# Optimization experiments

Hardware: AMD Instinct MI355X
Metric: run time of the kernel (lower is better)

Reference implementation:

```python
import jax, jax.numpy as jnp
import numpy as np

H = 5  # hidden size of both LSTMs

def _lstm_layer(x, Wih, Whh, bih, bhh):
    """x: [B,T,I] -> hs: [B,T,H]. PyTorch gate order i,f,g,o; zero init state."""
    B, T, _ = x.shape
    # precompute input contribution for all timesteps: [T,B,4H]
    xg = (jnp.einsum('bti,gi->btg', x, Wih) + bih + bhh).transpose(1, 0, 2)
    def step(carry, xg_t):
        h, c = carry
        g = xg_t + h @ Whh.T
        i, f, gg, o = jnp.split(g, 4, axis=-1)
        c = jax.nn.sigmoid(f) * c + jax.nn.sigmoid(i) * jnp.tanh(gg)
        h = jax.nn.sigmoid(o) * jnp.tanh(c)
        return (h, c), h
    h0 = jnp.zeros((B, H), x.dtype)
    (_, _), hs = jax.lax.scan(step, (h0, h0), xg)
    return hs.transpose(1, 0, 2)  # [B,T,H]

def setup_inputs() -> dict:
    key = jax.random.key(0)
    ks = jax.random.split(key, 32)
    B, T = 16384, 128
    def u(k, shape, fan):
        s = 1.0 / np.sqrt(fan)
        return jax.random.uniform(k, shape, jnp.float32, -s, s)
    inp = {
        'x1': jax.random.normal(ks[0], (B, T, 5), jnp.float32),
        'x2': jax.random.normal(ks[1], (B, T, 5), jnp.float32),
        # lstm1 (1 layer)
        'Wih1': u(ks[2], (4*H, 5), H), 'Whh1': u(ks[3], (4*H, H), H),
        'bih1': u(ks[4], (4*H,), H), 'bhh1': u(ks[5], (4*H,), H),
        # lstm2 layer 0
        'Wih2a': u(ks[6], (4*H, 5), H), 'Whh2a': u(ks[7], (4*H, H), H),
        'bih2a': u(ks[8], (4*H,), H), 'bhh2a': u(ks[9], (4*H,), H),
        # lstm2 layer 1
        'Wih2b': u(ks[10], (4*H, H), H), 'Whh2b': u(ks[11], (4*H, H), H),
        'bih2b': u(ks[12], (4*H,), H), 'bhh2b': u(ks[13], (4*H,), H),
        # FC stack 20->32->32->16->16->5
        'W1': u(ks[14], (32, 20), 20), 'b1': u(ks[15], (32,), 20),
        'W2': u(ks[16], (32, 32), 32), 'b2': u(ks[17], (32,), 32),
        'W3': u(ks[18], (16, 32), 32), 'b3': u(ks[19], (16,), 32),
        'W4': u(ks[20], (16, 16), 16), 'b4': u(ks[21], (16,), 16),
        'W5': u(ks[22], (5, 16), 16), 'b5': u(ks[23], (5,), 16),
    }
    return inp

def reference(x1, x2, Wih1, Whh1, bih1, bhh1, Wih2a, Whh2a, bih2a, bhh2a,
              Wih2b, Whh2b, bih2b, bhh2b, W1, b1, W2, b2, W3, b3, W4, b4, W5, b5):
    out1 = _lstm_layer(x1, Wih1, Whh1, bih1, bhh1)[:, -1, :]            # [B,5]
    h2 = _lstm_layer(x2, Wih2a, Whh2a, bih2a, bhh2a)                    # [B,T,5]
    out2 = _lstm_layer(h2, Wih2b, Whh2b, bih2b, bhh2b)[:, -1, :]        # [B,5]
    out = jnp.concatenate([x1[:, -1, :], x2[:, -1, :], out1, out2], axis=1)  # [B,20]
    out = jax.nn.relu(out @ W1.T + b1)
    out = jax.nn.relu(out @ W2.T + b2)
    out = jax.nn.relu(out @ W3.T + b3)
    out = jax.nn.relu(out @ W4.T + b4)
    return out @ W5.T + b5  # [B,5]
```

## Files before the change

### kernel.cpp

```cpp
#include <hip/hip_runtime.h>

#define DEV __device__ __forceinline__
#define KSIG (-1.442695041f)
#define KTANH (-2.885390082f)

typedef float f2 __attribute__((ext_vector_type(2)));

DEV float fexp2(float x) { return __builtin_amdgcn_exp2f(x); }
DEV float frcp(float x) { return __builtin_amdgcn_rcpf(x); }
DEV float bperm(int a, float x) {
  return __int_as_float(__builtin_amdgcn_ds_bpermute(a, __float_as_int(x)));
}
DEV f2 pkfma(f2 a, f2 b, f2 c) { return __builtin_elementwise_fma(a, b, c); }

struct CellP {
  f2 wx[4][2];
  f2 wh[4][2];
  float wx4[4], wh4[4];
  f2 b2[4];
};

DEV void load_cellP(CellP& W, int u, const float* __restrict__ Wih,
                    const float* __restrict__ Whh,
                    const float* __restrict__ bih,
                    const float* __restrict__ bhh) {
#pragma unroll
  for (int rt = 0; rt < 4; ++rt) {
    int row = 5 * rt + u;
    float kx = (rt == 2) ? KTANH : KSIG;
    W.wx[rt][0] = (f2){kx * Wih[row * 5 + 0], kx * Wih[row * 5 + 1]};
    W.wx[rt][1] = (f2){kx * Wih[row * 5 + 2], kx * Wih[row * 5 + 3]};
    W.wx4[rt] = kx * Wih[row * 5 + 4];
    W.wh[rt][0] = (f2){kx * Whh[row * 5 + 0], kx * Whh[row * 5 + 1]};
    W.wh[rt][1] = (f2){kx * Whh[row * 5 + 2], kx * Whh[row * 5 + 3]};
    W.wh4[rt] = kx * Whh[row * 5 + 4];
    W.b2[rt] = (f2){kx * (bih[row] + bhh[row]), 0.f};
  }
}

DEV float stepP(const CellP& W, const f2 xp[2], float x4, float hAll[5],
                float& c, const int bp[5]) {
  f2 hp0 = (f2){hAll[0], hAll[1]};
  f2 hp1 = (f2){hAll[2], hAll[3]};
  float acc[4];
#pragma unroll
  for (int rt = 0; rt < 4; ++rt) {
    f2 a2 = pkfma(W.wx[rt][0], xp[0], W.b2[rt]);
    a2 = pkfma(W.wx[rt][1], xp[1], a2);
    a2 = pkfma(W.wh[rt][0], hp0, a2);
    a2 = pkfma(W.wh[rt][1], hp1, a2);
    float a = a2.x + a2.y;
    a = fmaf(W.wx4[rt], x4, a);
    acc[rt] = fmaf(W.wh4[rt], hAll[4], a);
  }
  float gi = frcp(1.f + fexp2(acc[0]));
  float gf = frcp(1.f + fexp2(acc[1]));
  float gg = fmaf(2.f, frcp(1.f + fexp2(acc[2])), -1.f);
  float go = frcp(1.f + fexp2(acc[3]));
  c = fmaf(gf, c, gi * gg);
  float th = fmaf(2.f, frcp(1.f + fexp2(KTANH * c)), -1.f);
  float h = go * th;
#pragma unroll
  for (int u2 = 0; u2 < 5; ++u2) hAll[u2] = bperm(bp[u2], h);
  return h;
}

__global__ __launch_bounds__(192, 4) void rnn3w_kernel(
    const float* __restrict__ x1, const float* __restrict__ x2,
    const float* __restrict__ Wih1, const float* __restrict__ Whh1,
    const float* __restrict__ bih1, const float* __restrict__ bhh1,
    const float* __restrict__ Wih2a, const float* __restrict__ Whh2a,
    const float* __restrict__ bih2a, const float* __restrict__ bhh2a,
    const float* __restrict__ Wih2b, const float* __restrict__ Whh2b,
    const float* __restrict__ bih2b, const float* __restrict__ bhh2b,
    const float* __restrict__ W1, const float* __restrict__ b1,
    const float* __restrict__ W2, const float* __restrict__ b2,
    const float* __restrict__ W3, const float* __restrict__ b3,
    const float* __restrict__ W4, const float* __restrict__ b4,
    const float* __restrict__ W5, const float* __restrict__ b5,
    float* __restrict__ out, int B) {
  __shared__ float sH[2][64];
  __shared__ float sIn[12][20];
  __shared__ float sA[12][32];
  __shared__ float sB[12][32];

  const int tid = threadIdx.x;
  const int w = tid >> 6;
  const int l = tid & 63;
  const int g = l / 5;
  const int u = l - 5 * g;
  const bool act = (g < 12);
  const int el = act ? g : 11;
  const int eg = blockIdx.x * 12 + el;
  const int egc = (eg < B) ? eg : (B - 1);

  CellP W;
  if (w == 0)
    load_cellP(W, u, Wih1, Whh1, bih1, bhh1);
  else if (w == 1)
    load_cellP(W, u, Wih2a, Whh2a, bih2a, bhh2a);
  else
    load_cellP(W, u, Wih2b, Whh2b, bih2b, bhh2b);

  int bp[5];
#pragma unroll
  for (int u2 = 0; u2 < 5; ++u2) bp[u2] = (5 * g + u2) * 4;

  const float* px = ((w == 0) ? x1 : x2) + (size_t)egc * 640;

  if (tid < 128) sH[tid >> 6][tid & 63] = 0.f;

  float hAll[5];
  float c = 0.f, hOwn = 0.f;
#pragma unroll
  for (int k = 0; k < 5; ++k) hAll[k] = 0.f;

  f2 xp[2];
  float x4 = 0.f;
  if (w < 2) {
    xp[0] = (f2){px[0], px[1]};
    xp[1] = (f2){px[2], px[3]};
    x4 = px[4];
  }
  __syncthreads();

  for (int t = 0; t < 128; ++t) {
    f2 xin[2];
    float xin4;
    if (w == 2) {
      const float* s = &sH[(t + 1) & 1][g * 5];
      xin[0] = (f2){s[0], s[1]};
      xin[1] = (f2){s[2], s[3]};
      xin4 = s[4];
    } else {
      xin[0] = xp[0];
      xin[1] = xp[1];
      xin4 = x4;
    }
    if (w < 2) {
      const int tn = (t < 127) ? t + 1 : 127;
      xp[0] = (f2){px[tn * 5 + 0], px[tn * 5 + 1]};
      xp[1] = (f2){px[tn * 5 + 2], px[tn * 5 + 3]};
      x4 = px[tn * 5 + 4];
    }
    hOwn = stepP(W, xin, xin4, hAll, c, bp);
    if (w == 2 && t == 0) {
#pragma unroll
      for (int k = 0; k < 5; ++k) hAll[k] = 0.f;
      c = 0.f;
      hOwn = 0.f;
    }
    if (w == 1 && act) sH[t & 1][g * 5 + u] = hOwn;
    __syncthreads();
  }

  if (w == 2) {
    const float* s = &sH[1][g * 5];
    f2 xin[2] = {(f2){s[0], s[1]}, (f2){s[2], s[3]}};
    hOwn = stepP(W, xin, s[4], hAll, c, bp);
  }

  if (act) {
    if (w == 0) {
      sIn[el][u] = x1[(size_t)egc * 640 + 635 + u];
      sIn[el][10 + u] = hOwn;
    } else if (w == 1) {
      sIn[el][5 + u] = x2[(size_t)egc * 640 + 635 + u];
    } else {
      sIn[el][15 + u] = hOwn;
    }
  }
  __syncthreads();

  for (int task = tid; task < 12 * 32; task += 192) {
    int e = task >> 5, n = task & 31;
    float acc = b1[n];
#pragma unroll
    for (int k = 0; k < 20; ++k) acc = fmaf(W1[n * 20 + k], sIn[e][k], acc);
    sA[e][n] = fmaxf(acc, 0.f);
  }
  __syncthreads();
  for (int task = tid; task < 12 * 32; task += 192) {
    int e = task >> 5, n = task & 31;
    float acc = b2[n];
#pragma unroll
    for (int k = 0; k < 32; ++k) acc = fmaf(W2[n * 32 + k], sA[e][k], acc);
    sB[e][n] = fmaxf(acc, 0.f);
  }
  __syncthreads();
  {
    int e = tid >> 4, n = tid & 15;
    float acc = b3[n];
#pragma unroll
    for (int k = 0; k < 32; ++k) acc = fmaf(W3[n * 32 + k], sB[e][k], acc);
    sA[e][n] = fmaxf(acc, 0.f);
  }
  __syncthreads();
  {
    int e = tid >> 4, n = tid & 15;
    float acc = b4[n];
#pragma unroll
    for (int k = 0; k < 16; ++k) acc = fmaf(W4[n * 16 + k], sA[e][k], acc);
    sB[e][n] = fmaxf(acc, 0.f);
  }
  __syncthreads();
  if (tid < 60) {
    int e = tid / 5, n = tid - 5 * (tid / 5);
    float acc = b5[n];
#pragma unroll
    for (int k = 0; k < 16; ++k) acc = fmaf(W5[n * 16 + k], sB[e][k], acc);
    int ego = blockIdx.x * 12 + e;
    if (ego < B) out[(size_t)ego * 5 + n] = acc;
  }
}

extern "C" void kernel_launch(void* const* d_in, const int* in_sizes, int n_in,
                              void* d_out, int out_size, void* d_ws,
                              size_t ws_size, hipStream_t stream) {
  const float* x1 = (const float*)d_in[0];
  const float* x2 = (const float*)d_in[1];
  const float* Wih1 = (const float*)d_in[2];
  const float* Whh1 = (const float*)d_in[3];
  const float* bih1 = (const float*)d_in[4];
  const float* bhh1 = (const float*)d_in[5];
  const float* Wih2a = (const float*)d_in[6];
  const float* Whh2a = (const float*)d_in[7];
  const float* bih2a = (const float*)d_in[8];
  const float* bhh2a = (const float*)d_in[9];
  const float* Wih2b = (const float*)d_in[10];
  const float* Whh2b = (const float*)d_in[11];
  const float* bih2b = (const float*)d_in[12];
  const float* bhh2b = (const float*)d_in[13];
  const float* W1 = (const float*)d_in[14];
  const float* b1 = (const float*)d_in[15];
  const float* W2 = (const float*)d_in[16];
  const float* b2 = (const float*)d_in[17];
  const float* W3 = (const float*)d_in[18];
  const float* b3 = (const float*)d_in[19];
  const float* W4 = (const float*)d_in[20];
  const float* b4 = (const float*)d_in[21];
  const float* W5 = (const float*)d_in[22];
  const float* b5 = (const float*)d_in[23];

  int B = in_sizes[0] / 640;
  int nB = (B + 11) / 12;

  rnn3w_kernel<<<nB, 192, 0, stream>>>(
      x1, x2, Wih1, Whh1, bih1, bhh1, Wih2a, Whh2a, bih2a, bhh2a, Wih2b, Whh2b,
      bih2b, bhh2b, W1, b1, W2, b2, W3, b3, W4, b4, W5, b5, (float*)d_out, B);
}
```

Before: 224.3 us.

## Batch LSTM steps between barriers using 16-slot shared ring buffer

Replaces the per-timestep __syncthreads handshake between the layer-0 and layer-1 wavefronts with a 16-entry shared-memory ring of hidden states. Producers run 8 steps between barriers and the consumer wave lags one chunk behind, so there are 16 barriers instead of 128. Each wave now has its own specialised loop, which removes the per-step branches on wave id. The cost is a larger shared buffer and some extra pipeline fill and drain for the second layer.

```diff
diff --git a/kernel.cpp b/kernel.cpp
--- a/kernel.cpp
+++ b/kernel.cpp
@@ -65,7 +65,7 @@
   return h;
 }
 
-__global__ __launch_bounds__(192, 4) void rnn3w_kernel(
+__global__ __launch_bounds__(192, 4) void rnn_ring_kernel(
     const float* __restrict__ x1, const float* __restrict__ x2,
     const float* __restrict__ Wih1, const float* __restrict__ Whh1,
     const float* __restrict__ bih1, const float* __restrict__ bhh1,
@@ -79,7 +79,7 @@
     const float* __restrict__ W4, const float* __restrict__ b4,
     const float* __restrict__ W5, const float* __restrict__ b5,
     float* __restrict__ out, int B) {
-  __shared__ float sH[2][64];
+  __shared__ float sH[16][64];
   __shared__ float sIn[12][20];
   __shared__ float sA[12][32];
   __shared__ float sB[12][32];
@@ -94,81 +94,87 @@
   const int eg = blockIdx.x * 12 + el;
   const int egc = (eg < B) ? eg : (B - 1);
 
-  CellP W;
-  if (w == 0)
-    load_cellP(W, u, Wih1, Whh1, bih1, bhh1);
-  else if (w == 1)
-    load_cellP(W, u, Wih2a, Whh2a, bih2a, bhh2a);
-  else
-    load_cellP(W, u, Wih2b, Whh2b, bih2b, bhh2b);
-
   int bp[5];
 #pragma unroll
   for (int u2 = 0; u2 < 5; ++u2) bp[u2] = (5 * g + u2) * 4;
-
-  const float* px = ((w == 0) ? x1 : x2) + (size_t)egc * 640;
-
-  if (tid < 128) sH[tid >> 6][tid & 63] = 0.f;
 
   float hAll[5];
   float c = 0.f, hOwn = 0.f;
 #pragma unroll
   for (int k = 0; k < 5; ++k) hAll[k] = 0.f;
 
-  f2 xp[2];
-  float x4 = 0.f;
-  if (w < 2) {
-    xp[0] = (f2){px[0], px[1]};
-    xp[1] = (f2){px[2], px[3]};
-    x4 = px[4];
-  }
-  __syncthreads();
-
-  for (int t = 0; t < 128; ++t) {
-    f2 xin[2];
-    float xin4;
-    if (w == 2) {
-      const float* s = &sH[(t + 1) & 1][g * 5];
-      xin[0] = (f2){s[0], s[1]};
-      xin[1] = (f2){s[2], s[3]};
-      xin4 = s[4];
-    } else {
-      xin[0] = xp[0];
-      xin[1] = xp[1];
-      xin4 = x4;
-    }
-    if (w < 2) {
-      const int tn = (t < 127) ? t + 1 : 127;
-      xp[0] = (f2){px[tn * 5 + 0], px[tn * 5 + 1]};
-      xp[1] = (f2){px[tn * 5 + 2], px[tn * 5 + 3]};
-      x4 = px[tn * 5 + 4];
-    }
-    hOwn = stepP(W, xin, xin4, hAll, c, bp);
-    if (w == 2 && t == 0) {
-#pragma unroll
-      for (int k = 0; k < 5; ++k) hAll[k] = 0.f;
-      c = 0.f;
-      hOwn = 0.f;
-    }
-    if (w == 1 && act) sH[t & 1][g * 5 + u] = hOwn;
-    __syncthreads();
-  }
-
-  if (w == 2) {
-    const float* s = &sH[1][g * 5];
-    f2 xin[2] = {(f2){s[0], s[1]}, (f2){s[2], s[3]}};
-    hOwn = stepP(W, xin, s[4], hAll, c, bp);
-  }
-
-  if (act) {
-    if (w == 0) {
+  if (w == 0) {
+    CellP W;
+    load_cellP(W, u, Wih1, Whh1, bih1, bhh1);
+    const float* px = x1 + (size_t)egc * 640;
+    f2 xp[2] = {(f2){px[0], px[1]}, (f2){px[2], px[3]}};
+    float x4 = px[4];
+    for (int it = 0; it < 16; ++it) {
+#pragma unroll
+      for (int k = 0; k < 8; ++k) {
+        const int t = it * 8 + k;
+        const int tn = (t < 127) ? t + 1 : 127;
+        f2 n0 = (f2){px[tn * 5 + 0], px[tn * 5 + 1]};
+        f2 n1 = (f2){px[tn * 5 + 2], px[tn * 5 + 3]};
+        float n4 = px[tn * 5 + 4];
+        hOwn = stepP(W, xp, x4, hAll, c, bp);
+        xp[0] = n0;
+        xp[1] = n1;
+        x4 = n4;
+      }
+      __syncthreads();
+    }
+    if (act) {
       sIn[el][u] = x1[(size_t)egc * 640 + 635 + u];
       sIn[el][10 + u] = hOwn;
-    } else if (w == 1) {
-      sIn[el][5 + u] = x2[(size_t)egc * 640 + 635 + u];
-    } else {
-      sIn[el][15 + u] = hOwn;
-    }
+    }
+  } else if (w == 1) {
+    CellP W;
+    load_cellP(W, u, Wih2a, Whh2a, bih2a, bhh2a);
+    const float* px = x2 + (size_t)egc * 640;
+    f2 xp[2] = {(f2){px[0], px[1]}, (f2){px[2], px[3]}};
+    float x4 = px[4];
+    for (int it = 0; it < 16; ++it) {
+#pragma unroll
+      for (int k = 0; k < 8; ++k) {
+        const int t = it * 8 + k;
+        const int tn = (t < 127) ? t + 1 : 127;
+        f2 n0 = (f2){px[tn * 5 + 0], px[tn * 5 + 1]};
+        f2 n1 = (f2){px[tn * 5 + 2], px[tn * 5 + 3]};
+        float n4 = px[tn * 5 + 4];
+        hOwn = stepP(W, xp, x4, hAll, c, bp);
+        sH[t & 15][l] = hOwn;
+        xp[0] = n0;
+        xp[1] = n1;
+        x4 = n4;
+      }
+      __syncthreads();
+    }
+    if (act) sIn[el][5 + u] = x2[(size_t)egc * 640 + 635 + u];
+  } else {
+    CellP W;
+    load_cellP(W, u, Wih2b, Whh2b, bih2b, bhh2b);
+    const int sbase = g * 5;
+    for (int it = 0; it < 16; ++it) {
+      if (it > 0) {
+#pragma unroll
+        for (int k = 0; k < 8; ++k) {
+          const int t = (it - 1) * 8 + k;
+          const float* s = &sH[t & 15][sbase];
+          f2 xin[2] = {(f2){s[0], s[1]}, (f2){s[2], s[3]}};
+          hOwn = stepP(W, xin, s[4], hAll, c, bp);
+        }
+      }
+      __syncthreads();
+    }
+#pragma unroll
+    for (int k = 0; k < 8; ++k) {
+      const int t = 120 + k;
+      const float* s = &sH[t & 15][sbase];
+      f2 xin[2] = {(f2){s[0], s[1]}, (f2){s[2], s[3]}};
+      hOwn = stepP(W, xin, s[4], hAll, c, bp);
+    }
+    if (act) sIn[el][15 + u] = hOwn;
   }
   __syncthreads();
 
@@ -245,7 +251,7 @@
   int B = in_sizes[0] / 640;
   int nB = (B + 11) / 12;
 
-  rnn3w_kernel<<<nB, 192, 0, stream>>>(
+  rnn_ring_kernel<<<nB, 192, 0, stream>>>(
       x1, x2, Wih1, Whh1, bih1, bhh1, Wih2a, Whh2a, bih2a, bhh2a, Wih2b, Whh2b,
       bih2b, bhh2b, W1, b1, W2, b2, W3, b3, W4, b4, W5, b5, (float*)d_out, B);
 }
```

After: 233.6 us. +4.2%, slower.

## Process two interleaved sample groups per thread to raise ILP in LSTM recurrence

Applied to the files above, without the earlier changes.

Each thread now advances two independent batch elements (A and B) through the LSTM cell in lockstep, so every block handles 24 samples instead of 12 and launches half as many blocks. Interleaving the two independent dependency chains is meant to hide the latency of the serial exp/rcp/bpermute chain and to halve the per-timestep barrier cost per sample. The cost is roughly double the register pressure under the same launch bounds, which could cause spills or lower occupancy. The FC tail is widened to cover 24 samples.

```diff
diff --git a/kernel.cpp b/kernel.cpp
--- a/kernel.cpp
+++ b/kernel.cpp
@@ -38,34 +38,51 @@
   }
 }
 
-DEV float stepP(const CellP& W, const f2 xp[2], float x4, float hAll[5],
-                float& c, const int bp[5]) {
-  f2 hp0 = (f2){hAll[0], hAll[1]};
-  f2 hp1 = (f2){hAll[2], hAll[3]};
-  float acc[4];
+DEV void stepP2(const CellP& W, const f2 xA[2], float x4A, const f2 xB[2],
+                float x4B, float hA[5], float hB[5], float& cA, float& cB,
+                float& hOwnA, float& hOwnB, const int bp[5]) {
+  f2 hA0 = (f2){hA[0], hA[1]}, hA1 = (f2){hA[2], hA[3]};
+  f2 hB0 = (f2){hB[0], hB[1]}, hB1 = (f2){hB[2], hB[3]};
+  float accA[4], accB[4];
 #pragma unroll
   for (int rt = 0; rt < 4; ++rt) {
-    f2 a2 = pkfma(W.wx[rt][0], xp[0], W.b2[rt]);
-    a2 = pkfma(W.wx[rt][1], xp[1], a2);
-    a2 = pkfma(W.wh[rt][0], hp0, a2);
-    a2 = pkfma(W.wh[rt][1], hp1, a2);
-    float a = a2.x + a2.y;
-    a = fmaf(W.wx4[rt], x4, a);
-    acc[rt] = fmaf(W.wh4[rt], hAll[4], a);
-  }
-  float gi = frcp(1.f + fexp2(acc[0]));
-  float gf = frcp(1.f + fexp2(acc[1]));
-  float gg = fmaf(2.f, frcp(1.f + fexp2(acc[2])), -1.f);
-  float go = frcp(1.f + fexp2(acc[3]));
-  c = fmaf(gf, c, gi * gg);
-  float th = fmaf(2.f, frcp(1.f + fexp2(KTANH * c)), -1.f);
-  float h = go * th;
-#pragma unroll
-  for (int u2 = 0; u2 < 5; ++u2) hAll[u2] = bperm(bp[u2], h);
-  return h;
-}
-
-__global__ __launch_bounds__(192, 4) void rnn3w_kernel(
+    f2 a = pkfma(W.wx[rt][0], xA[0], W.b2[rt]);
+    f2 b = pkfma(W.wx[rt][0], xB[0], W.b2[rt]);
+    a = pkfma(W.wx[rt][1], xA[1], a);
+    b = pkfma(W.wx[rt][1], xB[1], b);
+    a = pkfma(W.wh[rt][0], hA0, a);
+    b = pkfma(W.wh[rt][0], hB0, b);
+    a = pkfma(W.wh[rt][1], hA1, a);
+    b = pkfma(W.wh[rt][1], hB1, b);
+    float sa = a.x + a.y;
+    float sb = b.x + b.y;
+    sa = fmaf(W.wx4[rt], x4A, sa);
+    sb = fmaf(W.wx4[rt], x4B, sb);
+    accA[rt] = fmaf(W.wh4[rt], hA[4], sa);
+    accB[rt] = fmaf(W.wh4[rt], hB[4], sb);
+  }
+  float giA = frcp(1.f + fexp2(accA[0]));
+  float giB = frcp(1.f + fexp2(accB[0]));
+  float gfA = frcp(1.f + fexp2(accA[1]));
+  float gfB = frcp(1.f + fexp2(accB[1]));
+  float ggA = fmaf(2.f, frcp(1.f + fexp2(accA[2])), -1.f);
+  float ggB = fmaf(2.f, frcp(1.f + fexp2(accB[2])), -1.f);
+  float goA = frcp(1.f + fexp2(accA[3]));
+  float goB = frcp(1.f + fexp2(accB[3]));
+  cA = fmaf(gfA, cA, giA * ggA);
+  cB = fmaf(gfB, cB, giB * ggB);
+  float thA = fmaf(2.f, frcp(1.f + fexp2(KTANH * cA)), -1.f);
+  float thB = fmaf(2.f, frcp(1.f + fexp2(KTANH * cB)), -1.f);
+  hOwnA = goA * thA;
+  hOwnB = goB * thB;
+#pragma unroll
+  for (int u2 = 0; u2 < 5; ++u2) {
+    hA[u2] = bperm(bp[u2], hOwnA);
+    hB[u2] = bperm(bp[u2], hOwnB);
+  }
+}
+
+__global__ __launch_bounds__(192, 4) void rnn2s_kernel(
     const float* __restrict__ x1, const float* __restrict__ x2,
     const float* __restrict__ Wih1, const float* __restrict__ Whh1,
     const float* __restrict__ bih1, const float* __restrict__ bhh1,
@@ -79,10 +96,10 @@
     const float* __restrict__ W4, const float* __restrict__ b4,
     const float* __restrict__ W5, const float* __restrict__ b5,
     float* __restrict__ out, int B) {
-  __shared__ float sH[2][64];
-  __shared__ float sIn[12][20];
-  __shared__ float sA[12][32];
-  __shared__ float sB[12][32];
+  __shared__ float sH[2][2][64];
+  __shared__ float sIn[24][20];
+  __shared__ float sA[24][32];
+  __shared__ float sB[24][32];
 
   const int tid = threadIdx.x;
   const int w = tid >> 6;
@@ -91,8 +108,10 @@
   const int u = l - 5 * g;
   const bool act = (g < 12);
   const int el = act ? g : 11;
-  const int eg = blockIdx.x * 12 + el;
-  const int egc = (eg < B) ? eg : (B - 1);
+  const int eA = blockIdx.x * 24 + el;
+  const int eB = eA + 12;
+  const int eAc = (eA < B) ? eA : (B - 1);
+  const int eBc = (eB < B) ? eB : (B - 1);
 
   CellP W;
   if (w == 0)
@@ -106,73 +125,96 @@
 #pragma unroll
   for (int u2 = 0; u2 < 5; ++u2) bp[u2] = (5 * g + u2) * 4;
 
-  const float* px = ((w == 0) ? x1 : x2) + (size_t)egc * 640;
-
-  if (tid < 128) sH[tid >> 6][tid & 63] = 0.f;
-
-  float hAll[5];
-  float c = 0.f, hOwn = 0.f;
-#pragma unroll
-  for (int k = 0; k < 5; ++k) hAll[k] = 0.f;
-
-  f2 xp[2];
-  float x4 = 0.f;
+  for (int i = tid; i < 256; i += 192) ((float*)sH)[i] = 0.f;
+
+  float hA[5], hB[5];
+  float cA = 0.f, cB = 0.f, hOwnA = 0.f, hOwnB = 0.f;
+#pragma unroll
+  for (int k = 0; k < 5; ++k) hA[k] = hB[k] = 0.f;
+
+  const float* pxA = ((w == 0) ? x1 : x2) + (size_t)eAc * 640;
+  const float* pxB = ((w == 0) ? x1 : x2) + (size_t)eBc * 640;
+
+  f2 xpA[2], xpB[2];
+  float x4A = 0.f, x4B = 0.f;
   if (w < 2) {
-    xp[0] = (f2){px[0], px[1]};
-    xp[1] = (f2){px[2], px[3]};
-    x4 = px[4];
+    xpA[0] = (f2){pxA[0], pxA[1]};
+    xpA[1] = (f2){pxA[2], pxA[3]};
+    x4A = pxA[4];
+    xpB[0] = (f2){pxB[0], pxB[1]};
+    xpB[1] = (f2){pxB[2], pxB[3]};
+    x4B = pxB[4];
   }
   __syncthreads();
 
   for (int t = 0; t < 128; ++t) {
-    f2 xin[2];
-    float xin4;
+    f2 xinA[2], xinB[2];
+    float xin4A, xin4B;
     if (w == 2) {
-      const float* s = &sH[(t + 1) & 1][g * 5];
-      xin[0] = (f2){s[0], s[1]};
-      xin[1] = (f2){s[2], s[3]};
-      xin4 = s[4];
+      const float* sa_ = &sH[(t + 1) & 1][0][g * 5];
+      const float* sb_ = &sH[(t + 1) & 1][1][g * 5];
+      xinA[0] = (f2){sa_[0], sa_[1]};
+      xinA[1] = (f2){sa_[2], sa_[3]};
+      xin4A = sa_[4];
+      xinB[0] = (f2){sb_[0], sb_[1]};
+      xinB[1] = (f2){sb_[2], sb_[3]};
+      xin4B = sb_[4];
     } else {
-      xin[0] = xp[0];
-      xin[1] = xp[1];
-      xin4 = x4;
+      xinA[0] = xpA[0];
+      xinA[1] = xpA[1];
+      xin4A = x4A;
+      xinB[0] = xpB[0];
+      xinB[1] = xpB[1];
+      xin4B = x4B;
     }
     if (w < 2) {
       const int tn = (t < 127) ? t + 1 : 127;
-      xp[0] = (f2){px[tn * 5 + 0], px[tn * 5 + 1]};
-      xp[1] = (f2){px[tn * 5 + 2], px[tn * 5 + 3]};
-      x4 = px[tn * 5 + 4];
-    }
-    hOwn = stepP(W, xin, xin4, hAll, c, bp);
+      xpA[0] = (f2){pxA[tn * 5 + 0], pxA[tn * 5 + 1]};
+      xpA[1] = (f2){pxA[tn * 5 + 2], pxA[tn * 5 + 3]};
+      x4A = pxA[tn * 5 + 4];
+      xpB[0] = (f2){pxB[tn * 5 + 0], pxB[tn * 5 + 1]};
+      xpB[1] = (f2){pxB[tn * 5 + 2], pxB[tn * 5 + 3]};
+      x4B = pxB[tn * 5 + 4];
+    }
+    stepP2(W, xinA, xin4A, xinB, xin4B, hA, hB, cA, cB, hOwnA, hOwnB, bp);
     if (w == 2 && t == 0) {
 #pragma unroll
-      for (int k = 0; k < 5; ++k) hAll[k] = 0.f;
-      c = 0.f;
-      hOwn = 0.f;
-    }
-    if (w == 1 && act) sH[t & 1][g * 5 + u] = hOwn;
+      for (int k = 0; k < 5; ++k) hA[k] = hB[k] = 0.f;
+      cA = cB = 0.f;
+      hOwnA = hOwnB = 0.f;
+    }
+    if (w == 1) {
+      sH[t & 1][0][l] = hOwnA;
+      sH[t & 1][1][l] = hOwnB;
+    }
     __syncthreads();
   }
 
   if (w == 2) {
-    const float* s = &sH[1][g * 5];
-    f2 xin[2] = {(f2){s[0], s[1]}, (f2){s[2], s[3]}};
-    hOwn = stepP(W, xin, s[4], hAll, c, bp);
+    const float* sa_ = &sH[1][0][g * 5];
+    const float* sb_ = &sH[1][1][g * 5];
+    f2 xinA[2] = {(f2){sa_[0], sa_[1]}, (f2){sa_[2], sa_[3]}};
+    f2 xinB[2] = {(f2){sb_[0], sb_[1]}, (f2){sb_[2], sb_[3]}};
+    stepP2(W, xinA, sa_[4], xinB, sb_[4], hA, hB, cA, cB, hOwnA, hOwnB, bp);
   }
 
   if (act) {
     if (w == 0) {
-      sIn[el][u] = x1[(size_t)egc * 640 + 635 + u];
-      sIn[el][10 + u] = hOwn;
+      sIn[el][u] = x1[(size_t)eAc * 640 + 635 + u];
+      sIn[el][10 + u] = hOwnA;
+      sIn[12 + el][u] = x1[(size_t)eBc * 640 + 635 + u];
+      sIn[12 + el][10 + u] = hOwnB;
     } else if (w == 1) {
-      sIn[el][5 + u] = x2[(size_t)egc * 640 + 635 + u];
+      sIn[el][5 + u] = x2[(size_t)eAc * 640 + 635 + u];
+      sIn[12 + el][5 + u] = x2[(size_t)eBc * 640 + 635 + u];
     } else {
-      sIn[el][15 + u] = hOwn;
-    }
-  }
-  __syncthreads();
-
-  for (int task = tid; task < 12 * 32; task += 192) {
+      sIn[el][15 + u] = hOwnA;
+      sIn[12 + el][15 + u] = hOwnB;
+    }
+  }
+  __syncthreads();
+
+  for (int task = tid; task < 24 * 32; task += 192) {
     int e = task >> 5, n = task & 31;
     float acc = b1[n];
 #pragma unroll
@@ -180,7 +222,7 @@
     sA[e][n] = fmaxf(acc, 0.f);
   }
   __syncthreads();
-  for (int task = tid; task < 12 * 32; task += 192) {
+  for (int task = tid; task < 24 * 32; task += 192) {
     int e = task >> 5, n = task & 31;
     float acc = b2[n];
 #pragma unroll
@@ -188,28 +230,28 @@
     sB[e][n] = fmaxf(acc, 0.f);
   }
   __syncthreads();
-  {
-    int e = tid >> 4, n = tid & 15;
+  for (int task = tid; task < 24 * 16; task += 192) {
+    int e = task >> 4, n = task & 15;
     float acc = b3[n];
 #pragma unroll
     for (int k = 0; k < 32; ++k) acc = fmaf(W3[n * 32 + k], sB[e][k], acc);
     sA[e][n] = fmaxf(acc, 0.f);
   }
   __syncthreads();
-  {
-    int e = tid >> 4, n = tid & 15;
+  for (int task = tid; task < 24 * 16; task += 192) {
+    int e = task >> 4, n = task & 15;
     float acc = b4[n];
 #pragma unroll
     for (int k = 0; k < 16; ++k) acc = fmaf(W4[n * 16 + k], sA[e][k], acc);
     sB[e][n] = fmaxf(acc, 0.f);
   }
   __syncthreads();
-  if (tid < 60) {
+  if (tid < 120) {
     int e = tid / 5, n = tid - 5 * (tid / 5);
     float acc = b5[n];
 #pragma unroll
     for (int k = 0; k < 16; ++k) acc = fmaf(W5[n * 16 + k], sB[e][k], acc);
-    int ego = blockIdx.x * 12 + e;
+    int ego = blockIdx.x * 24 + e;
     if (ego < B) out[(size_t)ego * 5 + n] = acc;
   }
 }
@@ -243,9 +285,9 @@
   const float* b5 = (const float*)d_in[23];
 
   int B = in_sizes[0] / 640;
-  int nB = (B + 11) / 12;
-
-  rnn3w_kernel<<<nB, 192, 0, stream>>>(
+  int nB = (B + 23) / 24;
+
+  rnn2s_kernel<<<nB, 192, 0, stream>>>(
       x1, x2, Wih1, Whh1, bih1, bhh1, Wih2a, Whh2a, bih2a, bhh2a, Wih2b, Whh2b,
       bih2b, bhh2b, W1, b1, W2, b2, W3, b3, W4, b4, W5, b5, (float*)d_out, B);
 }
```

After: 236.5 us. +5.5%, slower.
